# Performance work log

Measured on AMD Instinct MI355X. Metric: run time of the kernel, lower is better.

## Reference

```python
import jax, jax.numpy as jnp
import numpy as np

B, IN_F, OUT_F, KD = 256, 1024, 128, 16


def setup_inputs() -> dict:
    key = jax.random.key(0)
    k1, k2 = jax.random.split(key)
    x = jax.random.normal(k1, (B, IN_F), dtype=jnp.float32)
    t_mat = jax.random.normal(k2, (IN_F, OUT_F, KD), dtype=jnp.float32)
    return {"x": x, "t_mat": t_mat}


def reference(x, t_mat):
    # Projection: [B, in] @ [in, out*kd] -> [B, out, kd]
    m = jnp.einsum('bi,iok->bok', x, t_mat)
    # All-pairs L1 distance over kernel dim: [B, B, out]
    norm = jnp.sum(jnp.abs(m[:, None, :, :] - m[None, :, :, :]), axis=-1)
    # exp(-norm) summed over the partner axis; subtract 1 for self-pair (norm=0 -> exp=1)
    o_b = jnp.sum(jnp.exp(-norm), axis=1) - 1.0  # [B, out]
    return jnp.concatenate([x, o_b], axis=1)  # [B, in + out]
```

## Files before the change

kernel.cpp:

```cpp
#include <hip/hip_runtime.h>
#include <hip/hip_fp16.h>


#define BATCH 256
#define INF   1024
#define OUTF  128
#define KDIM  16
#define TCOLS 2048
#define OCOLS 1152
#define XB    1032

typedef __attribute__((ext_vector_type(8))) short short8;
typedef __attribute__((ext_vector_type(4))) float f32x4;

__device__ inline unsigned pack_bf2(float lo, float hi) {
    return __builtin_amdgcn_perm(__float_as_uint(hi), __float_as_uint(lo), 0x07060302u);
}
__device__ inline unsigned short bf_trunc(float f) {
    return (unsigned short)(__float_as_uint(f) >> 16);
}

__global__ __launch_bounds__(256) void k_gemm(const float* __restrict__ x,
                                              const float* __restrict__ T,
                                              __half* __restrict__ mh) {
    const int blk = blockIdx.x;
    const int o   = blk & 127;
    const int mq  = blk >> 7;
    const int tid = threadIdx.x;
    const int wave = tid >> 6, lane = tid & 63;
    const int l15 = lane & 15, q = lane >> 4;

    __shared__ unsigned short bs[16][XB];
    __shared__ __half pmout[64][16];

    {
        const int kb = tid >> 2, n0 = (tid & 3) * 4;
        #pragma unroll
        for (int pass = 0; pass < 16; ++pass) {
            const int k = pass * 64 + kb;
            float4 v = *reinterpret_cast<const float4*>(&T[k * TCOLS + o * KDIM + n0]);
            bs[n0 + 0][k] = bf_trunc(v.x);
            bs[n0 + 1][k] = bf_trunc(v.y);
            bs[n0 + 2][k] = bf_trunc(v.z);
            bs[n0 + 3][k] = bf_trunc(v.w);
        }
    }
    __syncthreads();

    const int mt = mq * 4 + wave;
    f32x4 acc = {0.f, 0.f, 0.f, 0.f};
    const float* xr = &x[(mt * 16 + l15) * INF + q * 8];
    #pragma unroll 8
    for (int ks = 0; ks < 32; ++ks) {
        const int k0 = ks * 32;
        short8 bfr = *reinterpret_cast<const short8*>(&bs[l15][k0 + q * 8]);
        float4 a0 = *reinterpret_cast<const float4*>(xr + k0);
        float4 a1 = *reinterpret_cast<const float4*>(xr + k0 + 4);
        union { unsigned u[4]; short8 s; } ua;
        ua.u[0] = pack_bf2(a0.x, a0.y); ua.u[1] = pack_bf2(a0.z, a0.w);
        ua.u[2] = pack_bf2(a1.x, a1.y); ua.u[3] = pack_bf2(a1.z, a1.w);
        acc = __builtin_amdgcn_mfma_f32_16x16x32_bf16(ua.s, bfr, acc, 0, 0, 0);
    }

    #pragma unroll
    for (int r = 0; r < 4; ++r)
        pmout[wave * 16 + q * 4 + r][l15] = __float2half(acc[r]);
    __syncthreads();

    if (tid < 128) {
        const int row = tid >> 1, hh = tid & 1;
        uint4 v = *reinterpret_cast<const uint4*>(&pmout[row][hh * 8]);
        *reinterpret_cast<uint4*>(&mh[o * (BATCH * KDIM) + (mq * 64 + row) * KDIM + hh * 8]) = v;
    }
}

__global__ __launch_bounds__(1024) void k_pair(const float* __restrict__ x,
                                               const __half* __restrict__ mh,
                                               float* __restrict__ out) {
    const int blk = blockIdx.x;
    const int o   = blk & 127;
    const int h   = blk >> 7;
    const int tid = threadIdx.x;

    __shared__ __half2 pm[BATCH][8];
    __shared__ float part[1024];

    if (tid < 256)
        reinterpret_cast<float4*>(out)[blk * 288 + tid] =
            reinterpret_cast<const float4*>(x)[blk * 256 + tid];

    if (tid < 512) {
        uint4 v = *reinterpret_cast<const uint4*>(
            &mh[o * (BATCH * KDIM) + (tid >> 1) * KDIM + (tid & 1) * 8]);
        *reinterpret_cast<uint4*>(&pm[tid >> 1][(tid & 1) * 4]) = v;
    }
    __syncthreads();

    const int i1 = tid & 127;
    const int b1 = h * 128 + i1;
    const int bsel = tid >> 7;
    __half2 my[8];
    {
        union { uint4 u[2]; __half2 hh[8]; } c;
        c.u[0] = *reinterpret_cast<const uint4*>(&pm[b1][0]);
        c.u[1] = *reinterpret_cast<const uint4*>(&pm[b1][4]);
        #pragma unroll
        for (int j = 0; j < 8; ++j) my[j] = c.hh[j];
    }
    float tot = 0.f;
    const int b2_lo = bsel * 32;
    #pragma unroll 4
    for (int b2 = b2_lo; b2 < b2_lo + 32; ++b2) {
        union { uint4 u[2]; __half2 hh[8]; } co;
        co.u[0] = *reinterpret_cast<const uint4*>(&pm[b2][0]);
        co.u[1] = *reinterpret_cast<const uint4*>(&pm[b2][4]);
        __half2 e0 = __float2half2_rn(0.f), e1 = __float2half2_rn(0.f);
        __half2 e2 = __float2half2_rn(0.f), e3 = __float2half2_rn(0.f);
        #pragma unroll
        for (int j = 0; j < 2; ++j) {
            e0 = __hadd2(e0, __habs2(__hsub2(my[j],     co.hh[j])));
            e1 = __hadd2(e1, __habs2(__hsub2(my[j + 2], co.hh[j + 2])));
            e2 = __hadd2(e2, __habs2(__hsub2(my[j + 4], co.hh[j + 4])));
            e3 = __hadd2(e3, __habs2(__hsub2(my[j + 6], co.hh[j + 6])));
        }
        __half2 es = __hadd2(__hadd2(e0, e1), __hadd2(e2, e3));
        float n = __low2float(es) + __high2float(es);
        tot += __expf(-n);
    }
    part[bsel * 128 + i1] = tot;
    __syncthreads();

    if (tid < 128) {
        float s = -1.0f;
        #pragma unroll
        for (int j = 0; j < 8; ++j) s += part[j * 128 + tid];
        out[(h * 128 + tid) * OCOLS + INF + o] = s;
    }
}

extern "C" void kernel_launch(void* const* d_in, const int* in_sizes, int n_in,
                              void* d_out, int out_size, void* d_ws, size_t ws_size,
                              hipStream_t stream) {
    const float* x = (const float*)d_in[0];
    const float* T = (const float*)d_in[1];
    float* out = (float*)d_out;
    __half* mh = (__half*)d_ws;

    k_gemm<<<512, 256, 0, stream>>>(x, T, mh);
    k_pair<<<256, 1024, 0, stream>>>(x, mh, out);
}
```

Before: 88.53 us.

## Register-block pair kernel over 4 rows and prefetch x in GEMM

The pairwise kernel now has each thread hold 4 query rows in registers and loop over 8 partners, so each partner row read from LDS is reused four times and the partner-axis split widens from 8 to 32. The final reduction grows to 32 partials per output. The GEMM kernel adds a 4-deep register prefetch of x rows, fully unrolls the k loop, and sets an occupancy hint of 2 blocks. Register pressure rises in both kernels, which may reduce occupancy.

Result: no change. 87.89 us (-0.7%).

```diff
diff --git a/kernel.cpp b/kernel.cpp
--- a/kernel.cpp
+++ b/kernel.cpp
@@ -20,9 +20,9 @@
     return (unsigned short)(__float_as_uint(f) >> 16);
 }
 
-__global__ __launch_bounds__(256) void k_gemm(const float* __restrict__ x,
-                                              const float* __restrict__ T,
-                                              __half* __restrict__ mh) {
+__global__ __launch_bounds__(256, 2) void k_gemm(const float* __restrict__ x,
+                                                 const float* __restrict__ T,
+                                                 __half* __restrict__ mh) {
     const int blk = blockIdx.x;
     const int o   = blk & 127;
     const int mq  = blk >> 7;
@@ -48,14 +48,23 @@
     __syncthreads();
 
     const int mt = mq * 4 + wave;
+    const float* xr = &x[(mt * 16 + l15) * INF + q * 8];
+
+    float4 st[4][2];
+    #pragma unroll
+    for (int p = 0; p < 4; ++p) {
+        st[p][0] = *reinterpret_cast<const float4*>(xr + p * 32);
+        st[p][1] = *reinterpret_cast<const float4*>(xr + p * 32 + 4);
+    }
     f32x4 acc = {0.f, 0.f, 0.f, 0.f};
-    const float* xr = &x[(mt * 16 + l15) * INF + q * 8];
-    #pragma unroll 8
+    #pragma unroll
     for (int ks = 0; ks < 32; ++ks) {
-        const int k0 = ks * 32;
-        short8 bfr = *reinterpret_cast<const short8*>(&bs[l15][k0 + q * 8]);
-        float4 a0 = *reinterpret_cast<const float4*>(xr + k0);
-        float4 a1 = *reinterpret_cast<const float4*>(xr + k0 + 4);
+        const int p = ks & 3;
+        float4 a0 = st[p][0], a1 = st[p][1];
+        const int kn = (ks + 4 < 32) ? ks + 4 : ks;
+        st[p][0] = *reinterpret_cast<const float4*>(xr + kn * 32);
+        st[p][1] = *reinterpret_cast<const float4*>(xr + kn * 32 + 4);
+        short8 bfr = *reinterpret_cast<const short8*>(&bs[l15][ks * 32 + q * 8]);
         union { unsigned u[4]; short8 s; } ua;
         ua.u[0] = pack_bf2(a0.x, a0.y); ua.u[1] = pack_bf2(a0.z, a0.w);
         ua.u[2] = pack_bf2(a1.x, a1.y); ua.u[3] = pack_bf2(a1.z, a1.w);
@@ -83,7 +92,7 @@
     const int tid = threadIdx.x;
 
     __shared__ __half2 pm[BATCH][8];
-    __shared__ float part[1024];
+    __shared__ float part[32][128];
 
     if (tid < 256)
         reinterpret_cast<float4*>(out)[blk * 288 + tid] =
@@ -96,44 +105,49 @@
     }
     __syncthreads();
 
-    const int i1 = tid & 127;
-    const int b1 = h * 128 + i1;
-    const int bsel = tid >> 7;
-    __half2 my[8];
-    {
+    const int i1 = tid & 31;
+    const int bsel = tid >> 5;
+    __half2 my[4][8];
+    #pragma unroll
+    for (int r = 0; r < 4; ++r) {
         union { uint4 u[2]; __half2 hh[8]; } c;
-        c.u[0] = *reinterpret_cast<const uint4*>(&pm[b1][0]);
-        c.u[1] = *reinterpret_cast<const uint4*>(&pm[b1][4]);
+        c.u[0] = *reinterpret_cast<const uint4*>(&pm[h * 128 + r * 32 + i1][0]);
+        c.u[1] = *reinterpret_cast<const uint4*>(&pm[h * 128 + r * 32 + i1][4]);
         #pragma unroll
-        for (int j = 0; j < 8; ++j) my[j] = c.hh[j];
+        for (int j = 0; j < 8; ++j) my[r][j] = c.hh[j];
     }
-    float tot = 0.f;
-    const int b2_lo = bsel * 32;
-    #pragma unroll 4
-    for (int b2 = b2_lo; b2 < b2_lo + 32; ++b2) {
+
+    float tot[4] = {0.f, 0.f, 0.f, 0.f};
+    const int b2_lo = bsel * 8;
+    #pragma unroll
+    for (int b2 = b2_lo; b2 < b2_lo + 8; ++b2) {
         union { uint4 u[2]; __half2 hh[8]; } co;
         co.u[0] = *reinterpret_cast<const uint4*>(&pm[b2][0]);
         co.u[1] = *reinterpret_cast<const uint4*>(&pm[b2][4]);
-        __half2 e0 = __float2half2_rn(0.f), e1 = __float2half2_rn(0.f);
-        __half2 e2 = __float2half2_rn(0.f), e3 = __float2half2_rn(0.f);
         #pragma unroll
-        for (int j = 0; j < 2; ++j) {
-            e0 = __hadd2(e0, __habs2(__hsub2(my[j],     co.hh[j])));
-            e1 = __hadd2(e1, __habs2(__hsub2(my[j + 2], co.hh[j + 2])));
-            e2 = __hadd2(e2, __habs2(__hsub2(my[j + 4], co.hh[j + 4])));
-            e3 = __hadd2(e3, __habs2(__hsub2(my[j + 6], co.hh[j + 6])));
+        for (int r = 0; r < 4; ++r) {
+            __half2 e0 = __habs2(__hsub2(my[r][0], co.hh[0]));
+            __half2 e1 = __habs2(__hsub2(my[r][1], co.hh[1]));
+            __half2 e2 = __habs2(__hsub2(my[r][2], co.hh[2]));
+            __half2 e3 = __habs2(__hsub2(my[r][3], co.hh[3]));
+            e0 = __hadd2(e0, __habs2(__hsub2(my[r][4], co.hh[4])));
+            e1 = __hadd2(e1, __habs2(__hsub2(my[r][5], co.hh[5])));
+            e2 = __hadd2(e2, __habs2(__hsub2(my[r][6], co.hh[6])));
+            e3 = __hadd2(e3, __habs2(__hsub2(my[r][7], co.hh[7])));
+            __half2 es = __hadd2(__hadd2(e0, e1), __hadd2(e2, e3));
+            float n = __low2float(es) + __high2float(es);
+            tot[r] += __expf(-n);
         }
-        __half2 es = __hadd2(__hadd2(e0, e1), __hadd2(e2, e3));
-        float n = __low2float(es) + __high2float(es);
-        tot += __expf(-n);
     }
-    part[bsel * 128 + i1] = tot;
+    #pragma unroll
+    for (int r = 0; r < 4; ++r)
+        part[bsel][r * 32 + i1] = tot[r];
     __syncthreads();
 
     if (tid < 128) {
         float s = -1.0f;
         #pragma unroll
-        for (int j = 0; j < 8; ++j) s += part[j * 128 + tid];
+        for (int j = 0; j < 32; ++j) s += part[j][tid];
         out[(h * 128 + tid) * OCOLS + INF + o] = s;
     }
 }
```
